# Optimization experiments

Hardware: AMD Instinct MI355X
Metric: run time of the kernel (lower is better)

The kernel has to match this reference:

```python
import jax, jax.numpy as jnp
import numpy as np

MASKED = True


def setup_inputs() -> dict:
    key = jax.random.key(0)
    kq, kk, kv = jax.random.split(key, 3)
    shape = (4, 16, 2048, 64)  # [B, H, S, d]
    q = jax.random.normal(kq, shape, dtype=jnp.float32)
    k = jax.random.normal(kk, shape, dtype=jnp.float32)
    v = jax.random.normal(kv, shape, dtype=jnp.float32)
    return {"q": q, "k": k, "v": v}


def reference(q, k, v):
    d = k.shape[-1]
    scale = 1.0 / jnp.sqrt(jnp.asarray(d, dtype=q.dtype))
    # [B, H, S, S]
    att = jnp.einsum("bhqd,bhkd->bhqk", q, k) * scale
    if MASKED:
        # Faithful to torch source: tril of the scores, then mask where zero
        tri = jnp.tril(att)
        att = jnp.where(tri == 0, -jnp.inf, att)
    att = jax.nn.softmax(att, axis=-1)
    return jnp.einsum("bhqk,bhkd->bhqd", att, v)
```

## Files before the change

### kernel.cpp

```cpp
#include <hip/hip_runtime.h>
#include <hip/hip_bf16.h>

typedef __attribute__((ext_vector_type(8)))  short bf16x8;
typedef __attribute__((ext_vector_type(4)))  float f32x4;
typedef __attribute__((ext_vector_type(16))) float f32x16;
typedef unsigned short ushort_t;

#define S_LEN 2048
#define D_DIM 64
#define FIXED_M 14.0f

#if __has_builtin(__builtin_amdgcn_exp2f)
#define EXP2(x) __builtin_amdgcn_exp2f(x)
#else
#define EXP2(x) __expf((x) * 0.6931471805599453f)
#endif

__device__ __forceinline__ short f2bf(float f) {
  union { float f; unsigned u; } x; x.f = f;
  unsigned r = x.u + 0x7fffu + ((x.u >> 16) & 1u);
  return (short)(r >> 16);
}

__device__ __forceinline__ unsigned cvtpk_bf16(float lo, float hi) {
  unsigned r;
  asm("v_cvt_pk_bf16_f32 %0, %1, %2" : "=v"(r) : "v"(lo), "v"(hi));
  return r;
}

__device__ __forceinline__ void pl32swap(unsigned& a, unsigned& b) {
  asm volatile("v_permlane32_swap_b32 %0, %1" : "+v"(a), "+v"(b));
}

__device__ __forceinline__ void gl_lds16(const ushort_t* g, ushort_t* l) {
  __builtin_amdgcn_global_load_lds(
      (const __attribute__((address_space(1))) unsigned*)g,
      (__attribute__((address_space(3))) unsigned*)l, 16, 0, 0);
}

__global__ void conv_bf16_kernel(const float* __restrict__ in,
                                 ushort_t* __restrict__ out, long n8) {
  long i = (long)blockIdx.x * blockDim.x + threadIdx.x;
  const long stride = (long)gridDim.x * blockDim.x;
  for (; i < n8; i += stride) {
    const float4* p = (const float4*)(in + i * 8);
    float4 a = p[0], b = p[1];
    bf16x8 t;
    t[0]=f2bf(a.x); t[1]=f2bf(a.y); t[2]=f2bf(a.z); t[3]=f2bf(a.w);
    t[4]=f2bf(b.x); t[5]=f2bf(b.y); t[6]=f2bf(b.z); t[7]=f2bf(b.w);
    *(bf16x8*)(out + i * 8) = t;
  }
}

__global__ void transpose_v_kernel(const float* __restrict__ V,
                                   ushort_t* __restrict__ Vt) {
  const int h  = blockIdx.x >> 5;
  const int s0 = (blockIdx.x & 31) * 64;
  const float* Vh = V + (size_t)h * S_LEN * D_DIM;
  ushort_t* Vth   = Vt + (size_t)h * D_DIM * S_LEN;
  __shared__ float tile[64][65];
  const int r  = threadIdx.x >> 2;
  const int c4 = (threadIdx.x & 3) * 16;
#pragma unroll
  for (int j = 0; j < 16; j += 4) {
    float4 x = *(const float4*)(Vh + (size_t)(s0 + r) * D_DIM + c4 + j);
    tile[r][c4 + j + 0] = x.x; tile[r][c4 + j + 1] = x.y;
    tile[r][c4 + j + 2] = x.z; tile[r][c4 + j + 3] = x.w;
  }
  __syncthreads();
  bf16x8 o0, o1;
#pragma unroll
  for (int j = 0; j < 8; ++j) o0[j] = f2bf(tile[c4 + j][r]);
#pragma unroll
  for (int j = 0; j < 8; ++j) o1[j] = f2bf(tile[c4 + 8 + j][r]);
  *(bf16x8*)(Vth + (size_t)r * S_LEN + s0 + c4)     = o0;
  *(bf16x8*)(Vth + (size_t)r * S_LEN + s0 + c4 + 8) = o1;
}

__global__ __launch_bounds__(256, 2)
void flash32_kernel(const float* __restrict__ Qf, const ushort_t* __restrict__ Kb,
                    const ushort_t* __restrict__ Vt, float* __restrict__ Og) {
  const int tid = threadIdx.x;
  const int l   = tid & 63;
  const int wv  = tid >> 6;
  const int hi  = l >> 5;
  const int l31 = l & 31;
  const int l7  = l & 7;
  const int l8  = l >> 3;

  const int bid  = blockIdx.x;
  const int r6   = bid & 63;
  const int head = (r6 & 7) * 8 + (r6 >> 3);
  const int g4   = bid >> 6;
  const int lo2  = g4 & 3;
  const int odd  = (g4 >> 2) & 1;
  const int top  = g4 >> 3;
  const int qidx = odd ? (top * 4 + lo2) : ((15 - top * 4) - lo2);
  const int q0   = qidx * 128;
  const int nt   = 2 * qidx + 2;

  const float*    Qh = Qf + (size_t)head * S_LEN * D_DIM;
  const ushort_t* Kh = Kb + (size_t)head * S_LEN * D_DIM;
  const ushort_t* Vh = Vt + (size_t)head * D_DIM * S_LEN;
  float*          Oh = Og + (size_t)head * S_LEN * D_DIM;

  __shared__ ushort_t smK[4][64 * 64];
  __shared__ ushort_t smV[4][64 * 64];

  const int qrow  = q0 + wv * 32 + l31;
  const int qminw = q0 + wv * 32;

  const int swsrc = (l7 ^ l8) * 8;
  const int rb    = l31 * 64;

#define STAGE_K(T) do {                                                    \
    const int kvk_ = (T) * 64;                                             \
    ushort_t* dst_ = smK[(T) & 3];                                         \
    _Pragma("unroll")                                                      \
    for (int u_ = 0; u_ < 2; ++u_) {                                       \
      const int idx_ = wv * 2 + u_;                                        \
      const int row_ = idx_ * 8 + l8;                                      \
      gl_lds16(Kh + (size_t)(kvk_ + row_) * 64 + swsrc,                    \
               dst_ + idx_ * 512);                                         \
    }                                                                      \
  } while (0)

#define STAGE_V(T) do {                                                    \
    const int kvv_ = (T) * 64;                                             \
    ushort_t* dst_ = smV[(T) & 3];                                         \
    _Pragma("unroll")                                                      \
    for (int u_ = 0; u_ < 2; ++u_) {                                       \
      const int idx_ = wv * 2 + u_;                                        \
      const int d_ = idx_ * 8 + l8;                                        \
      gl_lds16(Vh + (size_t)d_ * S_LEN + kvv_ + swsrc,                     \
               dst_ + idx_ * 512);                                         \
    }                                                                      \
  } while (0)

#define VMCNT0() asm volatile("s_waitcnt vmcnt(0)" ::: "memory")

#define QKT(S0, S1, T) do {                                                \
    _Pragma("unroll")                                                      \
    for (int i = 0; i < 16; ++i) { S0[i] = 0.f; S1[i] = 0.f; }             \
    const ushort_t* kb_ = smK[(T) & 3];                                    \
    __builtin_amdgcn_s_setprio(1);                                         \
    _Pragma("unroll")                                                      \
    for (int ks = 0; ks < 4; ++ks) {                                       \
      const int ch = ((ks * 2 + hi) ^ l7) * 8;                             \
      bf16x8 a0 = *(const bf16x8*)(kb_ + rb + ch);                         \
      bf16x8 a1 = *(const bf16x8*)(kb_ + 2048 + rb + ch);                  \
      S0 = __builtin_amdgcn_mfma_f32_32x32x16_bf16(a0, qf[ks], S0, 0, 0, 0); \
      S1 = __builtin_amdgcn_mfma_f32_32x32x16_bf16(a1, qf[ks], S1, 0, 0, 0); \
    }                                                                      \
    __builtin_amdgcn_s_setprio(0);                                         \
  } while (0)

#define SOFTMAX(S0, S1, KV0, PW) do {                                      \
    if ((KV0) + 63 > qminw) {                                              \
      _Pragma("unroll")                                                    \
      for (int r = 0; r < 16; ++r) {                                       \
        const int crow = (r & 3) + 8 * (r >> 2) + 4 * hi;                  \
        if ((KV0) + crow > qrow)      S0[r] = -INFINITY;                   \
        if ((KV0) + 32 + crow > qrow) S1[r] = -INFINITY;                   \
      }                                                                    \
    }                                                                      \
    _Pragma("unroll")                                                      \
    for (int i = 0; i < 16; ++i) S0[i] = EXP2(S0[i] - FIXED_M);            \
    _Pragma("unroll")                                                      \
    for (int i = 0; i < 16; ++i) S1[i] = EXP2(S1[i] - FIXED_M);            \
    float b8[8];                                                           \
    _Pragma("unroll")                                                      \
    for (int i = 0; i < 8; ++i)                                            \
      b8[i] = (S0[i] + S0[i+8]) + (S1[i] + S1[i+8]);                       \
    _Pragma("unroll")                                                      \
    for (int i = 0; i < 4; ++i) b8[i] += b8[i+4];                          \
    l_run += (b8[0] + b8[2]) + (b8[1] + b8[3]);                            \
    _Pragma("unroll")                                                      \
    for (int ks = 0; ks < 4; ++ks) {                                       \
      const int r0 = (ks & 1) * 8;                                         \
      unsigned w0, w1, w2, w3;                                             \
      if (ks < 2) {                                                        \
        w0 = cvtpk_bf16(S0[r0+0], S0[r0+1]); w2 = cvtpk_bf16(S0[r0+4], S0[r0+5]); \
        w1 = cvtpk_bf16(S0[r0+2], S0[r0+3]); w3 = cvtpk_bf16(S0[r0+6], S0[r0+7]); \
      } else {                                                             \
        w0 = cvtpk_bf16(S1[r0+0], S1[r0+1]); w2 = cvtpk_bf16(S1[r0+4], S1[r0+5]); \
        w1 = cvtpk_bf16(S1[r0+2], S1[r0+3]); w3 = cvtpk_bf16(S1[r0+6], S1[r0+7]); \
      }                                                                    \
      pl32swap(w0, w2); pl32swap(w1, w3);                                  \
      union { unsigned u[4]; bf16x8 v; } pu_;                              \
      pu_.u[0] = w0; pu_.u[1] = w1; pu_.u[2] = w2; pu_.u[3] = w3;          \
      PW[ks] = pu_.v;                                                      \
    }                                                                      \
  } while (0)

#define PV(T, PW) do {                                                     \
    const ushort_t* vb_ = smV[(T) & 3];                                    \
    __builtin_amdgcn_s_setprio(1);                                         \
    _Pragma("unroll")                                                      \
    for (int ks = 0; ks < 4; ++ks) {                                       \
      const int ch = ((ks * 2 + hi) ^ l7) * 8;                             \
      bf16x8 va  = *(const bf16x8*)(vb_ + rb + ch);                        \
      bf16x8 vB2 = *(const bf16x8*)(vb_ + 2048 + rb + ch);                 \
      accA = __builtin_amdgcn_mfma_f32_32x32x16_bf16(va,  PW[ks], accA, 0, 0, 0); \
      accB = __builtin_amdgcn_mfma_f32_32x32x16_bf16(vB2, PW[ks], accB, 0, 0, 0); \
    }                                                                      \
    __builtin_amdgcn_s_setprio(0);                                         \
  } while (0)

  STAGE_K(0);
  STAGE_V(0);
  STAGE_K(1);
  STAGE_V(1);

  bf16x8 qf[4];
  {
    const float sc = 0.125f * 1.44269504089f;
    const float* qp = Qh + (size_t)qrow * D_DIM + 8 * hi;
#pragma unroll
    for (int ks = 0; ks < 4; ++ks) {
      float4 x = *(const float4*)(qp + ks * 16);
      float4 y = *(const float4*)(qp + ks * 16 + 4);
      bf16x8 t;
      t[0]=f2bf(x.x*sc); t[1]=f2bf(x.y*sc);
      t[2]=f2bf(x.z*sc); t[3]=f2bf(x.w*sc);
      t[4]=f2bf(y.x*sc); t[5]=f2bf(y.y*sc);
      t[6]=f2bf(y.z*sc); t[7]=f2bf(y.w*sc);
      qf[ks] = t;
    }
  }

  f32x16 accA, accB, sA0, sA1, sB0, sB1;
#pragma unroll
  for (int i = 0; i < 16; ++i) { accA[i] = 0.f; accB[i] = 0.f; }
  float l_run = 0.f;
  bf16x8 pwA[4], pwB[4];

  VMCNT0();
  __builtin_amdgcn_s_barrier();

  for (int t = 0; t < nt; t += 2) {
    if (t + 2 < nt) {
      STAGE_K(t + 2);
      STAGE_V(t + 2);
      STAGE_K(t + 3);
      STAGE_V(t + 3);
    }
    QKT(sA0, sA1, t);
    QKT(sB0, sB1, t + 1);
    SOFTMAX(sA0, sA1, t * 64, pwA);
    SOFTMAX(sB0, sB1, (t + 1) * 64, pwB);
    PV(t, pwA);
    PV(t + 1, pwB);
    VMCNT0();
    __builtin_amdgcn_s_barrier();
  }

#undef STAGE_K
#undef STAGE_V
#undef VMCNT0
#undef QKT
#undef SOFTMAX
#undef PV

  l_run += __shfl_xor(l_run, 32, 64);
  const float inv = 1.0f / l_run;
  float* op = Oh + (size_t)qrow * D_DIM + 4 * hi;
#pragma unroll
  for (int m4 = 0; m4 < 4; ++m4) {
    float4 a = { accA[4*m4+0]*inv, accA[4*m4+1]*inv,
                 accA[4*m4+2]*inv, accA[4*m4+3]*inv };
    *(float4*)(op + 8 * m4) = a;
    float4 b = { accB[4*m4+0]*inv, accB[4*m4+1]*inv,
                 accB[4*m4+2]*inv, accB[4*m4+3]*inv };
    *(float4*)(op + 32 + 8 * m4) = b;
  }
}

#define BQ 64
#define BK 64
#define LDK 72
#define LDP 72

__device__ __forceinline__ unsigned pack_bf(float lo, float hi) {
  return (unsigned)(unsigned short)f2bf(lo) |
         ((unsigned)(unsigned short)f2bf(hi) << 16);
}

__global__ __launch_bounds__(256, 2)
void flash_fwd_kernel(const float* __restrict__ Qg, const float* __restrict__ Kg,
                      const float* __restrict__ Vg, float* __restrict__ Og) {
  const int tid  = threadIdx.x;
  const int lane = tid & 63;
  const int wv   = tid >> 6;
  const int grp  = lane >> 4;
  const int l16  = lane & 15;
  const int bid = blockIdx.x;
  const int qb  = 31 - (bid & 31);
  const int bh  = bid >> 5;
  const int q0  = qb * BQ;
  const size_t hoff = (size_t)bh * S_LEN * D_DIM;
  const float* Qh = Qg + hoff;
  const float* Kh = Kg + hoff;
  const float* Vh = Vg + hoff;
  float*       Oh = Og + hoff;
  __shared__ short sK [BK][LDK];
  __shared__ short sVT[D_DIM][LDP];
  __shared__ short sP [4][16][LDP];
  bf16x8 qf[2];
  {
    const float* qrow = Qh + (size_t)(q0 + wv*16 + l16) * D_DIM + grp*8;
#pragma unroll
    for (int kc = 0; kc < 2; ++kc) {
      float4 a = *reinterpret_cast<const float4*>(qrow + kc*32);
      float4 b = *reinterpret_cast<const float4*>(qrow + kc*32 + 4);
      bf16x8 t;
      t[0]=f2bf(a.x*0.125f); t[1]=f2bf(a.y*0.125f);
      t[2]=f2bf(a.z*0.125f); t[3]=f2bf(a.w*0.125f);
      t[4]=f2bf(b.x*0.125f); t[5]=f2bf(b.y*0.125f);
      t[6]=f2bf(b.z*0.125f); t[7]=f2bf(b.w*0.125f);
      qf[kc] = t;
    }
  }
  f32x4 acc[4];
#pragma unroll
  for (int nb = 0; nb < 4; ++nb) acc[nb] = (f32x4){0.f, 0.f, 0.f, 0.f};
  float m_i[4] = {-INFINITY, -INFINITY, -INFINITY, -INFINITY};
  float l_i[4] = {0.f, 0.f, 0.f, 0.f};
  const int srow = tid >> 2;
  const int scb  = tid & 3;
  for (int kt = 0; kt <= qb; ++kt) {
    const int kv0 = kt * BK;
    __syncthreads();
    {
      const float* src = Kh + (size_t)(kv0 + srow) * D_DIM + scb*16;
      float4 x0 = *reinterpret_cast<const float4*>(src);
      float4 x1 = *reinterpret_cast<const float4*>(src + 4);
      float4 x2 = *reinterpret_cast<const float4*>(src + 8);
      float4 x3 = *reinterpret_cast<const float4*>(src + 12);
      bf16x8 lo, hi;
      lo[0]=f2bf(x0.x); lo[1]=f2bf(x0.y); lo[2]=f2bf(x0.z); lo[3]=f2bf(x0.w);
      lo[4]=f2bf(x1.x); lo[5]=f2bf(x1.y); lo[6]=f2bf(x1.z); lo[7]=f2bf(x1.w);
      hi[0]=f2bf(x2.x); hi[1]=f2bf(x2.y); hi[2]=f2bf(x2.z); hi[3]=f2bf(x2.w);
      hi[4]=f2bf(x3.x); hi[5]=f2bf(x3.y); hi[6]=f2bf(x3.z); hi[7]=f2bf(x3.w);
      *reinterpret_cast<bf16x8*>(&sK[srow][scb*16])     = lo;
      *reinterpret_cast<bf16x8*>(&sK[srow][scb*16 + 8]) = hi;
    }
    {
      const float* src = Vh + (size_t)(kv0 + scb*16) * D_DIM + srow;
      bf16x8 lo, hi;
#pragma unroll
      for (int j = 0; j < 8; ++j) lo[j] = f2bf(src[(size_t)j * D_DIM]);
#pragma unroll
      for (int j = 0; j < 8; ++j) hi[j] = f2bf(src[(size_t)(j + 8) * D_DIM]);
      *reinterpret_cast<bf16x8*>(&sVT[srow][scb*16])     = lo;
      *reinterpret_cast<bf16x8*>(&sVT[srow][scb*16 + 8]) = hi;
    }
    __syncthreads();
    f32x4 sc[4];
#pragma unroll
    for (int nb = 0; nb < 4; ++nb) {
      f32x4 c = (f32x4){0.f, 0.f, 0.f, 0.f};
#pragma unroll
      for (int kc = 0; kc < 2; ++kc) {
        bf16x8 kf = *reinterpret_cast<const bf16x8*>(&sK[nb*16 + l16][kc*32 + grp*8]);
        c = __builtin_amdgcn_mfma_f32_16x16x32_bf16(qf[kc], kf, c, 0, 0, 0);
      }
      sc[nb] = c;
    }
    const bool diag = (kt == qb);
#pragma unroll
    for (int r = 0; r < 4; ++r) {
      const int qi = wv*16 + grp*4 + r;
      float s0 = sc[0][r], s1 = sc[1][r], s2 = sc[2][r], s3 = sc[3][r];
      if (diag) {
        if (l16 +  0 > qi) s0 = -INFINITY;
        if (l16 + 16 > qi) s1 = -INFINITY;
        if (l16 + 32 > qi) s2 = -INFINITY;
        if (l16 + 48 > qi) s3 = -INFINITY;
      }
      float mx = fmaxf(fmaxf(s0, s1), fmaxf(s2, s3));
#pragma unroll
      for (int off = 8; off; off >>= 1)
        mx = fmaxf(mx, __shfl_xor(mx, off, 64));
      const float mn    = fmaxf(m_i[r], mx);
      const float alpha = __expf(m_i[r] - mn);
      const float p0 = __expf(s0 - mn);
      const float p1 = __expf(s1 - mn);
      const float p2 = __expf(s2 - mn);
      const float p3 = __expf(s3 - mn);
      float rs = (p0 + p1) + (p2 + p3);
#pragma unroll
      for (int off = 8; off; off >>= 1)
        rs += __shfl_xor(rs, off, 64);
      l_i[r] = l_i[r] * alpha + rs;
      m_i[r] = mn;
      acc[0][r] *= alpha; acc[1][r] *= alpha;
      acc[2][r] *= alpha; acc[3][r] *= alpha;
      const float n0 = __shfl_xor(p0, 1, 64);
      const float n1 = __shfl_xor(p1, 1, 64);
      const float n2 = __shfl_xor(p2, 1, 64);
      const float n3 = __shfl_xor(p3, 1, 64);
      if (!(lane & 1)) {
        const int prow = grp*4 + r;
        unsigned* base = reinterpret_cast<unsigned*>(&sP[wv][prow][l16]);
        base[0]  = pack_bf(p0, n0);
        base[8]  = pack_bf(p1, n1);
        base[16] = pack_bf(p2, n2);
        base[24] = pack_bf(p3, n3);
      }
    }
    bf16x8 pf[2];
#pragma unroll
    for (int kc = 0; kc < 2; ++kc)
      pf[kc] = *reinterpret_cast<const bf16x8*>(&sP[wv][l16][kc*32 + grp*8]);
#pragma unroll
    for (int nb = 0; nb < 4; ++nb) {
#pragma unroll
      for (int kc = 0; kc < 2; ++kc) {
        bf16x8 vf = *reinterpret_cast<const bf16x8*>(&sVT[l16 + 16*nb][kc*32 + grp*8]);
        acc[nb] = __builtin_amdgcn_mfma_f32_16x16x32_bf16(pf[kc], vf, acc[nb], 0, 0, 0);
      }
    }
  }
#pragma unroll
  for (int r = 0; r < 4; ++r) {
    const float inv = 1.0f / l_i[r];
    float* orow = Oh + (size_t)(q0 + wv*16 + grp*4 + r) * D_DIM + l16;
#pragma unroll
    for (int nb = 0; nb < 4; ++nb)
      orow[nb*16] = acc[nb][r] * inv;
  }
}

extern "C" void kernel_launch(void* const* d_in, const int* in_sizes, int n_in,
                              void* d_out, int out_size, void* d_ws, size_t ws_size,
                              hipStream_t stream) {
  (void)n_in; (void)out_size;
  const float* q = (const float*)d_in[0];
  const float* k = (const float*)d_in[1];
  const float* v = (const float*)d_in[2];
  float* o = (float*)d_out;
  const int bh = in_sizes[0] / (S_LEN * D_DIM);
  const size_t elems = (size_t)bh * S_LEN * D_DIM;

  if (ws_size >= elems * 2 * 2) {
    ushort_t* Kb = (ushort_t*)d_ws;
    ushort_t* Vt = Kb + elems;
    const long n8 = (long)(elems / 8);
    conv_bf16_kernel<<<2048, 256, 0, stream>>>(k, Kb, n8);
    transpose_v_kernel<<<bh * (S_LEN / 64), 256, 0, stream>>>(v, Vt);
    flash32_kernel<<<bh * (S_LEN / 128), 256, 0, stream>>>(q, Kb, Vt, o);
  } else {
    flash_fwd_kernel<<<bh * (S_LEN / BQ), 256, 0, stream>>>(q, k, v, o);
  }
}
```

Before: 80.86 us.

## Restructure flash kernel into paired causal tiles with software-pipelined QK/softmax/PV

Each block now has 2 waves (128 threads) and handles two 64-row query tiles, tile 31-p and tile p, one after the other, so every block does the same amount of causal work. LDS staging shrinks from 4 to 2 buffers. The loop is software-pipelined so that the next tile's QK^T MFMA runs while the current tile's softmax and PV run, with barriers in between. The fixed max offset is folded into the initial value of the score accumulator, which removes a subtract from the softmax. The trade-off is fewer waves per block, more barriers and serial segments, and the same grid count with half-size blocks.

```diff
diff --git a/kernel.cpp b/kernel.cpp
--- a/kernel.cpp
+++ b/kernel.cpp
@@ -77,7 +77,7 @@
   *(bf16x8*)(Vth + (size_t)r * S_LEN + s0 + c4 + 8) = o1;
 }
 
-__global__ __launch_bounds__(256, 2)
+__global__ __launch_bounds__(128, 2)
 void flash32_kernel(const float* __restrict__ Qf, const ushort_t* __restrict__ Kb,
                     const ushort_t* __restrict__ Vt, float* __restrict__ Og) {
   const int tid = threadIdx.x;
@@ -91,58 +91,52 @@
   const int bid  = blockIdx.x;
   const int r6   = bid & 63;
   const int head = (r6 & 7) * 8 + (r6 >> 3);
-  const int g4   = bid >> 6;
-  const int lo2  = g4 & 3;
-  const int odd  = (g4 >> 2) & 1;
-  const int top  = g4 >> 3;
-  const int qidx = odd ? (top * 4 + lo2) : ((15 - top * 4) - lo2);
-  const int q0   = qidx * 128;
-  const int nt   = 2 * qidx + 2;
+  const int p    = bid >> 6;
+  const int qa   = 31 - p;
+  const int qb   = p;
 
   const float*    Qh = Qf + (size_t)head * S_LEN * D_DIM;
   const ushort_t* Kh = Kb + (size_t)head * S_LEN * D_DIM;
   const ushort_t* Vh = Vt + (size_t)head * D_DIM * S_LEN;
   float*          Oh = Og + (size_t)head * S_LEN * D_DIM;
 
-  __shared__ ushort_t smK[4][64 * 64];
-  __shared__ ushort_t smV[4][64 * 64];
-
-  const int qrow  = q0 + wv * 32 + l31;
-  const int qminw = q0 + wv * 32;
+  __shared__ ushort_t smK[2][64 * 64];
+  __shared__ ushort_t smV[2][64 * 64];
 
   const int swsrc = (l7 ^ l8) * 8;
   const int rb    = l31 * 64;
 
 #define STAGE_K(T) do {                                                    \
     const int kvk_ = (T) * 64;                                             \
-    ushort_t* dst_ = smK[(T) & 3];                                         \
-    _Pragma("unroll")                                                      \
-    for (int u_ = 0; u_ < 2; ++u_) {                                       \
-      const int idx_ = wv * 2 + u_;                                        \
+    ushort_t* dstk_ = smK[(T) & 1];                                        \
+    _Pragma("unroll")                                                      \
+    for (int u_ = 0; u_ < 4; ++u_) {                                       \
+      const int idx_ = wv * 4 + u_;                                        \
       const int row_ = idx_ * 8 + l8;                                      \
       gl_lds16(Kh + (size_t)(kvk_ + row_) * 64 + swsrc,                    \
-               dst_ + idx_ * 512);                                         \
+               dstk_ + idx_ * 512);                                        \
     }                                                                      \
   } while (0)
 
 #define STAGE_V(T) do {                                                    \
     const int kvv_ = (T) * 64;                                             \
-    ushort_t* dst_ = smV[(T) & 3];                                         \
-    _Pragma("unroll")                                                      \
-    for (int u_ = 0; u_ < 2; ++u_) {                                       \
-      const int idx_ = wv * 2 + u_;                                        \
+    ushort_t* dstv_ = smV[(T) & 1];                                        \
+    _Pragma("unroll")                                                      \
+    for (int u_ = 0; u_ < 4; ++u_) {                                       \
+      const int idx_ = wv * 4 + u_;                                        \
       const int d_ = idx_ * 8 + l8;                                        \
       gl_lds16(Vh + (size_t)d_ * S_LEN + kvv_ + swsrc,                     \
-               dst_ + idx_ * 512);                                         \
+               dstv_ + idx_ * 512);                                        \
     }                                                                      \
   } while (0)
 
 #define VMCNT0() asm volatile("s_waitcnt vmcnt(0)" ::: "memory")
+#define BAR()    __builtin_amdgcn_s_barrier()
 
 #define QKT(S0, S1, T) do {                                                \
     _Pragma("unroll")                                                      \
-    for (int i = 0; i < 16; ++i) { S0[i] = 0.f; S1[i] = 0.f; }             \
-    const ushort_t* kb_ = smK[(T) & 3];                                    \
+    for (int i = 0; i < 16; ++i) { S0[i] = -FIXED_M; S1[i] = -FIXED_M; }   \
+    const ushort_t* kb_ = smK[(T) & 1];                                    \
     __builtin_amdgcn_s_setprio(1);                                         \
     _Pragma("unroll")                                                      \
     for (int ks = 0; ks < 4; ++ks) {                                       \
@@ -155,7 +149,7 @@
     __builtin_amdgcn_s_setprio(0);                                         \
   } while (0)
 
-#define SOFTMAX(S0, S1, KV0, PW) do {                                      \
+#define SOFTMAX(S0, S1, KV0) do {                                          \
     if ((KV0) + 63 > qminw) {                                              \
       _Pragma("unroll")                                                    \
       for (int r = 0; r < 16; ++r) {                                       \
@@ -165,9 +159,9 @@
       }                                                                    \
     }                                                                      \
     _Pragma("unroll")                                                      \
-    for (int i = 0; i < 16; ++i) S0[i] = EXP2(S0[i] - FIXED_M);            \
-    _Pragma("unroll")                                                      \
-    for (int i = 0; i < 16; ++i) S1[i] = EXP2(S1[i] - FIXED_M);            \
+    for (int i = 0; i < 16; ++i) S0[i] = EXP2(S0[i]);                      \
+    _Pragma("unroll")                                                      \
+    for (int i = 0; i < 16; ++i) S1[i] = EXP2(S1[i]);                      \
     float b8[8];                                                           \
     _Pragma("unroll")                                                      \
     for (int i = 0; i < 8; ++i)                                            \
@@ -189,91 +183,116 @@
       pl32swap(w0, w2); pl32swap(w1, w3);                                  \
       union { unsigned u[4]; bf16x8 v; } pu_;                              \
       pu_.u[0] = w0; pu_.u[1] = w1; pu_.u[2] = w2; pu_.u[3] = w3;          \
-      PW[ks] = pu_.v;                                                      \
+      pw[ks] = pu_.v;                                                      \
     }                                                                      \
   } while (0)
 
-#define PV(T, PW) do {                                                     \
-    const ushort_t* vb_ = smV[(T) & 3];                                    \
+#define PV(T) do {                                                         \
+    const ushort_t* vb_ = smV[(T) & 1];                                    \
     __builtin_amdgcn_s_setprio(1);                                         \
     _Pragma("unroll")                                                      \
     for (int ks = 0; ks < 4; ++ks) {                                       \
       const int ch = ((ks * 2 + hi) ^ l7) * 8;                             \
       bf16x8 va  = *(const bf16x8*)(vb_ + rb + ch);                        \
       bf16x8 vB2 = *(const bf16x8*)(vb_ + 2048 + rb + ch);                 \
-      accA = __builtin_amdgcn_mfma_f32_32x32x16_bf16(va,  PW[ks], accA, 0, 0, 0); \
-      accB = __builtin_amdgcn_mfma_f32_32x32x16_bf16(vB2, PW[ks], accB, 0, 0, 0); \
+      accA = __builtin_amdgcn_mfma_f32_32x32x16_bf16(va,  pw[ks], accA, 0, 0, 0); \
+      accB = __builtin_amdgcn_mfma_f32_32x32x16_bf16(vB2, pw[ks], accB, 0, 0, 0); \
     }                                                                      \
     __builtin_amdgcn_s_setprio(0);                                         \
   } while (0)
 
-  STAGE_K(0);
-  STAGE_V(0);
-  STAGE_K(1);
-  STAGE_V(1);
-
-  bf16x8 qf[4];
-  {
-    const float sc = 0.125f * 1.44269504089f;
-    const float* qp = Qh + (size_t)qrow * D_DIM + 8 * hi;
-#pragma unroll
-    for (int ks = 0; ks < 4; ++ks) {
-      float4 x = *(const float4*)(qp + ks * 16);
-      float4 y = *(const float4*)(qp + ks * 16 + 4);
-      bf16x8 t;
-      t[0]=f2bf(x.x*sc); t[1]=f2bf(x.y*sc);
-      t[2]=f2bf(x.z*sc); t[3]=f2bf(x.w*sc);
-      t[4]=f2bf(y.x*sc); t[5]=f2bf(y.y*sc);
-      t[6]=f2bf(y.z*sc); t[7]=f2bf(y.w*sc);
-      qf[ks] = t;
-    }
-  }
-
-  f32x16 accA, accB, sA0, sA1, sB0, sB1;
-#pragma unroll
-  for (int i = 0; i < 16; ++i) { accA[i] = 0.f; accB[i] = 0.f; }
-  float l_run = 0.f;
-  bf16x8 pwA[4], pwB[4];
-
-  VMCNT0();
-  __builtin_amdgcn_s_barrier();
-
-  for (int t = 0; t < nt; t += 2) {
-    if (t + 2 < nt) {
+  for (int seg = 0; seg < 2; ++seg) {
+    const int qidx = seg ? qb : qa;
+    const int q0   = qidx * 64;
+    const int nt   = qidx + 1;
+
+    const int qrow  = q0 + wv * 32 + l31;
+    const int qminw = q0 + wv * 32;
+
+    if (seg) BAR();
+
+    STAGE_K(0);
+    STAGE_V(0);
+    STAGE_K(1);
+
+    bf16x8 qf[4];
+    {
+      const float sc = 0.125f * 1.44269504089f;
+      const float* qp = Qh + (size_t)qrow * D_DIM + 8 * hi;
+#pragma unroll
+      for (int ks = 0; ks < 4; ++ks) {
+        float4 x = *(const float4*)(qp + ks * 16);
+        float4 y = *(const float4*)(qp + ks * 16 + 4);
+        bf16x8 t;
+        t[0]=f2bf(x.x*sc); t[1]=f2bf(x.y*sc);
+        t[2]=f2bf(x.z*sc); t[3]=f2bf(x.w*sc);
+        t[4]=f2bf(y.x*sc); t[5]=f2bf(y.y*sc);
+        t[6]=f2bf(y.z*sc); t[7]=f2bf(y.w*sc);
+        qf[ks] = t;
+      }
+    }
+
+    f32x16 accA, accB, sA0, sA1, sB0, sB1;
+#pragma unroll
+    for (int i = 0; i < 16; ++i) { accA[i] = 0.f; accB[i] = 0.f; }
+    float l_run = 0.f;
+    bf16x8 pw[4];
+
+    VMCNT0();
+    BAR();
+    QKT(sA0, sA1, 0);
+
+    int t = 0;
+    for (; t + 2 < nt; t += 2) {
+      VMCNT0(); BAR();
       STAGE_K(t + 2);
+      STAGE_V(t + 1);
+      QKT(sB0, sB1, t + 1);
+      SOFTMAX(sA0, sA1, t * 64);
+      PV(t);
+      VMCNT0(); BAR();
+      if (t + 3 < nt) STAGE_K(t + 3);
       STAGE_V(t + 2);
-      STAGE_K(t + 3);
-      STAGE_V(t + 3);
-    }
-    QKT(sA0, sA1, t);
-    QKT(sB0, sB1, t + 1);
-    SOFTMAX(sA0, sA1, t * 64, pwA);
-    SOFTMAX(sB0, sB1, (t + 1) * 64, pwB);
-    PV(t, pwA);
-    PV(t + 1, pwB);
-    VMCNT0();
-    __builtin_amdgcn_s_barrier();
+      QKT(sA0, sA1, t + 2);
+      SOFTMAX(sB0, sB1, (t + 1) * 64);
+      PV(t + 1);
+    }
+    if (nt - t == 2) {
+      VMCNT0(); BAR();
+      STAGE_V(t + 1);
+      QKT(sB0, sB1, t + 1);
+      SOFTMAX(sA0, sA1, t * 64);
+      PV(t);
+      VMCNT0(); BAR();
+      SOFTMAX(sB0, sB1, (t + 1) * 64);
+      PV(t + 1);
+    } else {
+      VMCNT0(); BAR();
+      SOFTMAX(sA0, sA1, t * 64);
+      PV(t);
+    }
+
+    l_run += __shfl_xor(l_run, 32, 64);
+    const float inv = 1.0f / l_run;
+    float* op = Oh + (size_t)qrow * D_DIM + 4 * hi;
+#pragma unroll
+    for (int m4 = 0; m4 < 4; ++m4) {
+      float4 a = { accA[4*m4+0]*inv, accA[4*m4+1]*inv,
+                   accA[4*m4+2]*inv, accA[4*m4+3]*inv };
+      *(float4*)(op + 8 * m4) = a;
+      float4 b = { accB[4*m4+0]*inv, accB[4*m4+1]*inv,
+                   accB[4*m4+2]*inv, accB[4*m4+3]*inv };
+      *(float4*)(op + 32 + 8 * m4) = b;
+    }
   }
 
 #undef STAGE_K
 #undef STAGE_V
 #undef VMCNT0
+#undef BAR
 #undef QKT
 #undef SOFTMAX
 #undef PV
-
-  l_run += __shfl_xor(l_run, 32, 64);
-  const float inv = 1.0f / l_run;
-  float* op = Oh + (size_t)qrow * D_DIM + 4 * hi;
-#pragma unroll
-  for (int m4 = 0; m4 < 4; ++m4) {
-    float4 a = { accA[4*m4+0]*inv, accA[4*m4+1]*inv,
-                 accA[4*m4+2]*inv, accA[4*m4+3]*inv };
-    *(float4*)(op + 8 * m4) = a;
-    float4 b = { accB[4*m4+0]*inv, accB[4*m4+1]*inv,
-                 accB[4*m4+2]*inv, accB[4*m4+3]*inv };
-    *(float4*)(op + 32 + 8 * m4) = b;
-  }
 }
 
 #define BQ 64
@@ -449,7 +468,7 @@
     const long n8 = (long)(elems / 8);
     conv_bf16_kernel<<<2048, 256, 0, stream>>>(k, Kb, n8);
     transpose_v_kernel<<<bh * (S_LEN / 64), 256, 0, stream>>>(v, Vt);
-    flash32_kernel<<<bh * (S_LEN / 128), 256, 0, stream>>>(q, Kb, Vt, o);
+    flash32_kernel<<<bh * 16, 128, 0, stream>>>(q, Kb, Vt, o);
   } else {
     flash_fwd_kernel<<<bh * (S_LEN / BQ), 256, 0, stream>>>(q, k, v, o);
   }
```

Measured after the change: 78.42 us. -3.0%, faster.

## Replace LDS-staged 4-wave blocks with single-wave blocks loading K/V directly to registers

Applied to the files above, without the earlier changes.

The flash kernel now launches one 64-thread wave per block, each covering 32 query rows, instead of 256-thread blocks covering 128 rows that shared K/V tiles staged in LDS through global_load_lds. Each wave loads its K and V MFMA fragments straight from global memory into registers, double-buffering K across iterations, and drops all LDS use and barriers. The fixed max offset is folded into the score accumulator's initial value. This removes barrier and LDS traffic and adds many more independent blocks, but each wave now fetches K/V itself, so global/L2 traffic rises roughly fourfold and V loads are no longer prefetched ahead of use.

```diff
diff --git a/kernel.cpp b/kernel.cpp
--- a/kernel.cpp
+++ b/kernel.cpp
@@ -30,12 +30,6 @@
 
 __device__ __forceinline__ void pl32swap(unsigned& a, unsigned& b) {
   asm volatile("v_permlane32_swap_b32 %0, %1" : "+v"(a), "+v"(b));
-}
-
-__device__ __forceinline__ void gl_lds16(const ushort_t* g, ushort_t* l) {
-  __builtin_amdgcn_global_load_lds(
-      (const __attribute__((address_space(1))) unsigned*)g,
-      (__attribute__((address_space(3))) unsigned*)l, 16, 0, 0);
 }
 
 __global__ void conv_bf16_kernel(const float* __restrict__ in,
@@ -77,86 +71,67 @@
   *(bf16x8*)(Vth + (size_t)r * S_LEN + s0 + c4 + 8) = o1;
 }
 
-__global__ __launch_bounds__(256, 2)
+__global__ __launch_bounds__(64, 2)
 void flash32_kernel(const float* __restrict__ Qf, const ushort_t* __restrict__ Kb,
                     const ushort_t* __restrict__ Vt, float* __restrict__ Og) {
-  const int tid = threadIdx.x;
-  const int l   = tid & 63;
-  const int wv  = tid >> 6;
+  const int l   = threadIdx.x & 63;
   const int hi  = l >> 5;
   const int l31 = l & 31;
-  const int l7  = l & 7;
-  const int l8  = l >> 3;
 
   const int bid  = blockIdx.x;
   const int r6   = bid & 63;
   const int head = (r6 & 7) * 8 + (r6 >> 3);
-  const int g4   = bid >> 6;
-  const int lo2  = g4 & 3;
-  const int odd  = (g4 >> 2) & 1;
-  const int top  = g4 >> 3;
-  const int qidx = odd ? (top * 4 + lo2) : ((15 - top * 4) - lo2);
-  const int q0   = qidx * 128;
-  const int nt   = 2 * qidx + 2;
+  const int qidx = 63 - (bid >> 6);
+  const int q0   = qidx * 32;
+  const int nt   = ((qidx * 32 + 31) >> 6) + 1;
 
   const float*    Qh = Qf + (size_t)head * S_LEN * D_DIM;
   const ushort_t* Kh = Kb + (size_t)head * S_LEN * D_DIM;
   const ushort_t* Vh = Vt + (size_t)head * D_DIM * S_LEN;
   float*          Oh = Og + (size_t)head * S_LEN * D_DIM;
 
-  __shared__ ushort_t smK[4][64 * 64];
-  __shared__ ushort_t smV[4][64 * 64];
-
-  const int qrow  = q0 + wv * 32 + l31;
-  const int qminw = q0 + wv * 32;
-
-  const int swsrc = (l7 ^ l8) * 8;
-  const int rb    = l31 * 64;
-
-#define STAGE_K(T) do {                                                    \
-    const int kvk_ = (T) * 64;                                             \
-    ushort_t* dst_ = smK[(T) & 3];                                         \
-    _Pragma("unroll")                                                      \
-    for (int u_ = 0; u_ < 2; ++u_) {                                       \
-      const int idx_ = wv * 2 + u_;                                        \
-      const int row_ = idx_ * 8 + l8;                                      \
-      gl_lds16(Kh + (size_t)(kvk_ + row_) * 64 + swsrc,                    \
-               dst_ + idx_ * 512);                                         \
-    }                                                                      \
+  const int qrow = q0 + l31;
+
+#define LOADK(F, T) do {                                                   \
+    const ushort_t* kp_ = Kh + (size_t)((T) * 64 + l31) * 64 + hi * 8;     \
+    F[0] = *(const bf16x8*)(kp_);                                          \
+    F[1] = *(const bf16x8*)(kp_ + 16);                                     \
+    F[2] = *(const bf16x8*)(kp_ + 32);                                     \
+    F[3] = *(const bf16x8*)(kp_ + 48);                                     \
+    const ushort_t* kq_ = kp_ + 32 * 64;                                   \
+    F[4] = *(const bf16x8*)(kq_);                                          \
+    F[5] = *(const bf16x8*)(kq_ + 16);                                     \
+    F[6] = *(const bf16x8*)(kq_ + 32);                                     \
+    F[7] = *(const bf16x8*)(kq_ + 48);                                     \
   } while (0)
 
-#define STAGE_V(T) do {                                                    \
-    const int kvv_ = (T) * 64;                                             \
-    ushort_t* dst_ = smV[(T) & 3];                                         \
-    _Pragma("unroll")                                                      \
-    for (int u_ = 0; u_ < 2; ++u_) {                                       \
-      const int idx_ = wv * 2 + u_;                                        \
-      const int d_ = idx_ * 8 + l8;                                        \
-      gl_lds16(Vh + (size_t)d_ * S_LEN + kvv_ + swsrc,                     \
-               dst_ + idx_ * 512);                                         \
-    }                                                                      \
+#define LOADV(T) do {                                                      \
+    const ushort_t* vp_ = Vh + (size_t)l31 * S_LEN + (T) * 64 + hi * 8;    \
+    vv[0] = *(const bf16x8*)(vp_);                                         \
+    vv[1] = *(const bf16x8*)(vp_ + 16);                                    \
+    vv[2] = *(const bf16x8*)(vp_ + 32);                                    \
+    vv[3] = *(const bf16x8*)(vp_ + 48);                                    \
+    const ushort_t* vq_ = vp_ + (size_t)32 * S_LEN;                        \
+    vv[4] = *(const bf16x8*)(vq_);                                         \
+    vv[5] = *(const bf16x8*)(vq_ + 16);                                    \
+    vv[6] = *(const bf16x8*)(vq_ + 32);                                    \
+    vv[7] = *(const bf16x8*)(vq_ + 48);                                    \
   } while (0)
 
-#define VMCNT0() asm volatile("s_waitcnt vmcnt(0)" ::: "memory")
-
-#define QKT(S0, S1, T) do {                                                \
-    _Pragma("unroll")                                                      \
-    for (int i = 0; i < 16; ++i) { S0[i] = 0.f; S1[i] = 0.f; }             \
-    const ushort_t* kb_ = smK[(T) & 3];                                    \
+#define QKT(F) do {                                                        \
+    _Pragma("unroll")                                                      \
+    for (int i = 0; i < 16; ++i) { S0[i] = -FIXED_M; S1[i] = -FIXED_M; }   \
     __builtin_amdgcn_s_setprio(1);                                         \
     _Pragma("unroll")                                                      \
     for (int ks = 0; ks < 4; ++ks) {                                       \
-      const int ch = ((ks * 2 + hi) ^ l7) * 8;                             \
-      bf16x8 a0 = *(const bf16x8*)(kb_ + rb + ch);                         \
-      bf16x8 a1 = *(const bf16x8*)(kb_ + 2048 + rb + ch);                  \
-      S0 = __builtin_amdgcn_mfma_f32_32x32x16_bf16(a0, qf[ks], S0, 0, 0, 0); \
-      S1 = __builtin_amdgcn_mfma_f32_32x32x16_bf16(a1, qf[ks], S1, 0, 0, 0); \
+      S0 = __builtin_amdgcn_mfma_f32_32x32x16_bf16(F[ks],     qf[ks], S0, 0, 0, 0); \
+      S1 = __builtin_amdgcn_mfma_f32_32x32x16_bf16(F[ks + 4], qf[ks], S1, 0, 0, 0); \
     }                                                                      \
     __builtin_amdgcn_s_setprio(0);                                         \
   } while (0)
 
-#define SOFTMAX(S0, S1, KV0, PW) do {                                      \
-    if ((KV0) + 63 > qminw) {                                              \
+#define SOFTMAX(KV0) do {                                                  \
+    if ((KV0) + 63 > q0) {                                                 \
       _Pragma("unroll")                                                    \
       for (int r = 0; r < 16; ++r) {                                       \
         const int crow = (r & 3) + 8 * (r >> 2) + 4 * hi;                  \
@@ -165,9 +140,9 @@
       }                                                                    \
     }                                                                      \
     _Pragma("unroll")                                                      \
-    for (int i = 0; i < 16; ++i) S0[i] = EXP2(S0[i] - FIXED_M);            \
-    _Pragma("unroll")                                                      \
-    for (int i = 0; i < 16; ++i) S1[i] = EXP2(S1[i] - FIXED_M);            \
+    for (int i = 0; i < 16; ++i) S0[i] = EXP2(S0[i]);                      \
+    _Pragma("unroll")                                                      \
+    for (int i = 0; i < 16; ++i) S1[i] = EXP2(S1[i]);                      \
     float b8[8];                                                           \
     _Pragma("unroll")                                                      \
     for (int i = 0; i < 8; ++i)                                            \
@@ -189,28 +164,19 @@
       pl32swap(w0, w2); pl32swap(w1, w3);                                  \
       union { unsigned u[4]; bf16x8 v; } pu_;                              \
       pu_.u[0] = w0; pu_.u[1] = w1; pu_.u[2] = w2; pu_.u[3] = w3;          \
-      PW[ks] = pu_.v;                                                      \
+      pw[ks] = pu_.v;                                                      \
     }                                                                      \
   } while (0)
 
-#define PV(T, PW) do {                                                     \
-    const ushort_t* vb_ = smV[(T) & 3];                                    \
+#define PV() do {                                                          \
     __builtin_amdgcn_s_setprio(1);                                         \
     _Pragma("unroll")                                                      \
     for (int ks = 0; ks < 4; ++ks) {                                       \
-      const int ch = ((ks * 2 + hi) ^ l7) * 8;                             \
-      bf16x8 va  = *(const bf16x8*)(vb_ + rb + ch);                        \
-      bf16x8 vB2 = *(const bf16x8*)(vb_ + 2048 + rb + ch);                 \
-      accA = __builtin_amdgcn_mfma_f32_32x32x16_bf16(va,  PW[ks], accA, 0, 0, 0); \
-      accB = __builtin_amdgcn_mfma_f32_32x32x16_bf16(vB2, PW[ks], accB, 0, 0, 0); \
+      accA = __builtin_amdgcn_mfma_f32_32x32x16_bf16(vv[ks],     pw[ks], accA, 0, 0, 0); \
+      accB = __builtin_amdgcn_mfma_f32_32x32x16_bf16(vv[ks + 4], pw[ks], accB, 0, 0, 0); \
     }                                                                      \
     __builtin_amdgcn_s_setprio(0);                                         \
   } while (0)
-
-  STAGE_K(0);
-  STAGE_V(0);
-  STAGE_K(1);
-  STAGE_V(1);
 
   bf16x8 qf[4];
   {
@@ -229,35 +195,38 @@
     }
   }
 
-  f32x16 accA, accB, sA0, sA1, sB0, sB1;
+  f32x16 accA, accB, S0, S1;
 #pragma unroll
   for (int i = 0; i < 16; ++i) { accA[i] = 0.f; accB[i] = 0.f; }
   float l_run = 0.f;
-  bf16x8 pwA[4], pwB[4];
-
-  VMCNT0();
-  __builtin_amdgcn_s_barrier();
-
-  for (int t = 0; t < nt; t += 2) {
-    if (t + 2 < nt) {
-      STAGE_K(t + 2);
-      STAGE_V(t + 2);
-      STAGE_K(t + 3);
-      STAGE_V(t + 3);
-    }
-    QKT(sA0, sA1, t);
-    QKT(sB0, sB1, t + 1);
-    SOFTMAX(sA0, sA1, t * 64, pwA);
-    SOFTMAX(sB0, sB1, (t + 1) * 64, pwB);
-    PV(t, pwA);
-    PV(t + 1, pwB);
-    VMCNT0();
-    __builtin_amdgcn_s_barrier();
-  }
-
-#undef STAGE_K
-#undef STAGE_V
-#undef VMCNT0
+  bf16x8 ka[8], kb2[8], vv[8], pw[4];
+
+  LOADK(ka, 0);
+
+  int t = 0;
+  while (true) {
+    {
+      const int kv0 = t * 64;
+      LOADV(t);
+      if (t + 1 < nt) LOADK(kb2, t + 1);
+      QKT(ka);
+      SOFTMAX(kv0);
+      PV();
+    }
+    if (++t >= nt) break;
+    {
+      const int kv0 = t * 64;
+      LOADV(t);
+      if (t + 1 < nt) LOADK(ka, t + 1);
+      QKT(kb2);
+      SOFTMAX(kv0);
+      PV();
+    }
+    if (++t >= nt) break;
+  }
+
+#undef LOADK
+#undef LOADV
 #undef QKT
 #undef SOFTMAX
 #undef PV
@@ -449,7 +418,7 @@
     const long n8 = (long)(elems / 8);
     conv_bf16_kernel<<<2048, 256, 0, stream>>>(k, Kb, n8);
     transpose_v_kernel<<<bh * (S_LEN / 64), 256, 0, stream>>>(v, Vt);
-    flash32_kernel<<<bh * (S_LEN / 128), 256, 0, stream>>>(q, Kb, Vt, o);
+    flash32_kernel<<<bh * 64, 64, 0, stream>>>(q, Kb, Vt, o);
   } else {
     flash_fwd_kernel<<<bh * (S_LEN / BQ), 256, 0, stream>>>(q, k, v, o);
   }
```

After: 149.8 us. +85.3%, slower.

## Pair causal query tiles per block and merge prep kernels into one launch

Applied to the files above, without the earlier changes.

Each attention block now processes two query tiles, one heavy (15-p) and one light (p), so every block does the same total causal work. The grid shrinks from 1024 to 512 blocks. The K conversion and V transpose are merged into a single prep kernel launch. The fixed max offset is folded into the accumulator initialisation, which removes one subtract per exp. The cost is less block-level parallelism and serial segments inside each block, and the fast path now also requires exactly 64 heads.

```diff
diff --git a/kernel.cpp b/kernel.cpp
--- a/kernel.cpp
+++ b/kernel.cpp
@@ -38,43 +38,44 @@
       (__attribute__((address_space(3))) unsigned*)l, 16, 0, 0);
 }
 
-__global__ void conv_bf16_kernel(const float* __restrict__ in,
-                                 ushort_t* __restrict__ out, long n8) {
-  long i = (long)blockIdx.x * blockDim.x + threadIdx.x;
-  const long stride = (long)gridDim.x * blockDim.x;
-  for (; i < n8; i += stride) {
-    const float4* p = (const float4*)(in + i * 8);
-    float4 a = p[0], b = p[1];
-    bf16x8 t;
-    t[0]=f2bf(a.x); t[1]=f2bf(a.y); t[2]=f2bf(a.z); t[3]=f2bf(a.w);
-    t[4]=f2bf(b.x); t[5]=f2bf(b.y); t[6]=f2bf(b.z); t[7]=f2bf(b.w);
-    *(bf16x8*)(out + i * 8) = t;
-  }
-}
-
-__global__ void transpose_v_kernel(const float* __restrict__ V,
-                                   ushort_t* __restrict__ Vt) {
-  const int h  = blockIdx.x >> 5;
-  const int s0 = (blockIdx.x & 31) * 64;
-  const float* Vh = V + (size_t)h * S_LEN * D_DIM;
-  ushort_t* Vth   = Vt + (size_t)h * D_DIM * S_LEN;
-  __shared__ float tile[64][65];
-  const int r  = threadIdx.x >> 2;
-  const int c4 = (threadIdx.x & 3) * 16;
-#pragma unroll
-  for (int j = 0; j < 16; j += 4) {
-    float4 x = *(const float4*)(Vh + (size_t)(s0 + r) * D_DIM + c4 + j);
-    tile[r][c4 + j + 0] = x.x; tile[r][c4 + j + 1] = x.y;
-    tile[r][c4 + j + 2] = x.z; tile[r][c4 + j + 3] = x.w;
-  }
-  __syncthreads();
-  bf16x8 o0, o1;
-#pragma unroll
-  for (int j = 0; j < 8; ++j) o0[j] = f2bf(tile[c4 + j][r]);
-#pragma unroll
-  for (int j = 0; j < 8; ++j) o1[j] = f2bf(tile[c4 + 8 + j][r]);
-  *(bf16x8*)(Vth + (size_t)r * S_LEN + s0 + c4)     = o0;
-  *(bf16x8*)(Vth + (size_t)r * S_LEN + s0 + c4 + 8) = o1;
+__global__ void prep_kernel(const float* __restrict__ Kf, const float* __restrict__ Vf,
+                            ushort_t* __restrict__ Kb, ushort_t* __restrict__ Vt) {
+  if (blockIdx.x < 2048) {
+    const long n8 = (long)64 * S_LEN * D_DIM / 8;
+    long i = (long)blockIdx.x * blockDim.x + threadIdx.x;
+    const long stride = (long)2048 * blockDim.x;
+    for (; i < n8; i += stride) {
+      const float4* p = (const float4*)(Kf + i * 8);
+      float4 a = p[0], b = p[1];
+      bf16x8 t;
+      t[0]=f2bf(a.x); t[1]=f2bf(a.y); t[2]=f2bf(a.z); t[3]=f2bf(a.w);
+      t[4]=f2bf(b.x); t[5]=f2bf(b.y); t[6]=f2bf(b.z); t[7]=f2bf(b.w);
+      *(bf16x8*)(Kb + i * 8) = t;
+    }
+  } else {
+    const int bid = blockIdx.x - 2048;
+    const int h  = bid >> 5;
+    const int s0 = (bid & 31) * 64;
+    const float* Vh = Vf + (size_t)h * S_LEN * D_DIM;
+    ushort_t* Vth   = Vt + (size_t)h * D_DIM * S_LEN;
+    __shared__ float tile[64][65];
+    const int r  = threadIdx.x >> 2;
+    const int c4 = (threadIdx.x & 3) * 16;
+#pragma unroll
+    for (int j = 0; j < 16; j += 4) {
+      float4 x = *(const float4*)(Vh + (size_t)(s0 + r) * D_DIM + c4 + j);
+      tile[r][c4 + j + 0] = x.x; tile[r][c4 + j + 1] = x.y;
+      tile[r][c4 + j + 2] = x.z; tile[r][c4 + j + 3] = x.w;
+    }
+    __syncthreads();
+    bf16x8 o0, o1;
+#pragma unroll
+    for (int j = 0; j < 8; ++j) o0[j] = f2bf(tile[c4 + j][r]);
+#pragma unroll
+    for (int j = 0; j < 8; ++j) o1[j] = f2bf(tile[c4 + 8 + j][r]);
+    *(bf16x8*)(Vth + (size_t)r * S_LEN + s0 + c4)     = o0;
+    *(bf16x8*)(Vth + (size_t)r * S_LEN + s0 + c4 + 8) = o1;
+  }
 }
 
 __global__ __launch_bounds__(256, 2)
@@ -91,13 +92,9 @@
   const int bid  = blockIdx.x;
   const int r6   = bid & 63;
   const int head = (r6 & 7) * 8 + (r6 >> 3);
-  const int g4   = bid >> 6;
-  const int lo2  = g4 & 3;
-  const int odd  = (g4 >> 2) & 1;
-  const int top  = g4 >> 3;
-  const int qidx = odd ? (top * 4 + lo2) : ((15 - top * 4) - lo2);
-  const int q0   = qidx * 128;
-  const int nt   = 2 * qidx + 2;
+  const int p    = bid >> 6;
+  const int qhiQ = 15 - p;
+  const int qloQ = p;
 
   const float*    Qh = Qf + (size_t)head * S_LEN * D_DIM;
   const ushort_t* Kh = Kb + (size_t)head * S_LEN * D_DIM;
@@ -107,41 +104,37 @@
   __shared__ ushort_t smK[4][64 * 64];
   __shared__ ushort_t smV[4][64 * 64];
 
-  const int qrow  = q0 + wv * 32 + l31;
-  const int qminw = q0 + wv * 32;
-
   const int swsrc = (l7 ^ l8) * 8;
   const int rb    = l31 * 64;
 
 #define STAGE_K(T) do {                                                    \
     const int kvk_ = (T) * 64;                                             \
-    ushort_t* dst_ = smK[(T) & 3];                                         \
+    ushort_t* dk_ = smK[(T) & 3];                                          \
     _Pragma("unroll")                                                      \
     for (int u_ = 0; u_ < 2; ++u_) {                                       \
       const int idx_ = wv * 2 + u_;                                        \
       const int row_ = idx_ * 8 + l8;                                      \
-      gl_lds16(Kh + (size_t)(kvk_ + row_) * 64 + swsrc,                    \
-               dst_ + idx_ * 512);                                         \
+      gl_lds16(Kh + (size_t)(kvk_ + row_) * 64 + swsrc, dk_ + idx_ * 512); \
     }                                                                      \
   } while (0)
 
 #define STAGE_V(T) do {                                                    \
     const int kvv_ = (T) * 64;                                             \
-    ushort_t* dst_ = smV[(T) & 3];                                         \
+    ushort_t* dv_ = smV[(T) & 3];                                          \
     _Pragma("unroll")                                                      \
     for (int u_ = 0; u_ < 2; ++u_) {                                       \
       const int idx_ = wv * 2 + u_;                                        \
       const int d_ = idx_ * 8 + l8;                                        \
-      gl_lds16(Vh + (size_t)d_ * S_LEN + kvv_ + swsrc,                     \
-               dst_ + idx_ * 512);                                         \
+      gl_lds16(Vh + (size_t)d_ * S_LEN + kvv_ + swsrc, dv_ + idx_ * 512);  \
     }                                                                      \
   } while (0)
 
 #define VMCNT0() asm volatile("s_waitcnt vmcnt(0)" ::: "memory")
+#define BAR()    __builtin_amdgcn_s_barrier()
 
 #define QKT(S0, S1, T) do {                                                \
     _Pragma("unroll")                                                      \
-    for (int i = 0; i < 16; ++i) { S0[i] = 0.f; S1[i] = 0.f; }             \
+    for (int i = 0; i < 16; ++i) { S0[i] = -FIXED_M; S1[i] = -FIXED_M; }   \
     const ushort_t* kb_ = smK[(T) & 3];                                    \
     __builtin_amdgcn_s_setprio(1);                                         \
     _Pragma("unroll")                                                      \
@@ -165,9 +158,9 @@
       }                                                                    \
     }                                                                      \
     _Pragma("unroll")                                                      \
-    for (int i = 0; i < 16; ++i) S0[i] = EXP2(S0[i] - FIXED_M);            \
-    _Pragma("unroll")                                                      \
-    for (int i = 0; i < 16; ++i) S1[i] = EXP2(S1[i] - FIXED_M);            \
+    for (int i = 0; i < 16; ++i) S0[i] = EXP2(S0[i]);                      \
+    _Pragma("unroll")                                                      \
+    for (int i = 0; i < 16; ++i) S1[i] = EXP2(S1[i]);                      \
     float b8[8];                                                           \
     _Pragma("unroll")                                                      \
     for (int i = 0; i < 8; ++i)                                            \
@@ -207,73 +200,83 @@
     __builtin_amdgcn_s_setprio(0);                                         \
   } while (0)
 
-  STAGE_K(0);
-  STAGE_V(0);
-  STAGE_K(1);
-  STAGE_V(1);
-
-  bf16x8 qf[4];
-  {
-    const float sc = 0.125f * 1.44269504089f;
-    const float* qp = Qh + (size_t)qrow * D_DIM + 8 * hi;
-#pragma unroll
-    for (int ks = 0; ks < 4; ++ks) {
-      float4 x = *(const float4*)(qp + ks * 16);
-      float4 y = *(const float4*)(qp + ks * 16 + 4);
-      bf16x8 t;
-      t[0]=f2bf(x.x*sc); t[1]=f2bf(x.y*sc);
-      t[2]=f2bf(x.z*sc); t[3]=f2bf(x.w*sc);
-      t[4]=f2bf(y.x*sc); t[5]=f2bf(y.y*sc);
-      t[6]=f2bf(y.z*sc); t[7]=f2bf(y.w*sc);
-      qf[ks] = t;
-    }
-  }
-
-  f32x16 accA, accB, sA0, sA1, sB0, sB1;
-#pragma unroll
-  for (int i = 0; i < 16; ++i) { accA[i] = 0.f; accB[i] = 0.f; }
-  float l_run = 0.f;
-  bf16x8 pwA[4], pwB[4];
-
-  VMCNT0();
-  __builtin_amdgcn_s_barrier();
-
-  for (int t = 0; t < nt; t += 2) {
-    if (t + 2 < nt) {
-      STAGE_K(t + 2);
-      STAGE_V(t + 2);
-      STAGE_K(t + 3);
-      STAGE_V(t + 3);
-    }
-    QKT(sA0, sA1, t);
-    QKT(sB0, sB1, t + 1);
-    SOFTMAX(sA0, sA1, t * 64, pwA);
-    SOFTMAX(sB0, sB1, (t + 1) * 64, pwB);
-    PV(t, pwA);
-    PV(t + 1, pwB);
+  for (int seg = 0; seg < 2; ++seg) {
+    const int qidx = seg ? qloQ : qhiQ;
+    const int q0   = qidx * 128;
+    const int nt   = 2 * qidx + 2;
+
+    const int qrow  = q0 + wv * 32 + l31;
+    const int qminw = q0 + wv * 32;
+
+    STAGE_K(0);
+    STAGE_V(0);
+    STAGE_K(1);
+    STAGE_V(1);
+
+    bf16x8 qf[4];
+    {
+      const float sc = 0.125f * 1.44269504089f;
+      const float* qp = Qh + (size_t)qrow * D_DIM + 8 * hi;
+#pragma unroll
+      for (int ks = 0; ks < 4; ++ks) {
+        float4 x = *(const float4*)(qp + ks * 16);
+        float4 y = *(const float4*)(qp + ks * 16 + 4);
+        bf16x8 t;
+        t[0]=f2bf(x.x*sc); t[1]=f2bf(x.y*sc);
+        t[2]=f2bf(x.z*sc); t[3]=f2bf(x.w*sc);
+        t[4]=f2bf(y.x*sc); t[5]=f2bf(y.y*sc);
+        t[6]=f2bf(y.z*sc); t[7]=f2bf(y.w*sc);
+        qf[ks] = t;
+      }
+    }
+
+    f32x16 accA, accB, sA0, sA1, sB0, sB1;
+#pragma unroll
+    for (int i = 0; i < 16; ++i) { accA[i] = 0.f; accB[i] = 0.f; }
+    float l_run = 0.f;
+    bf16x8 pwA[4], pwB[4];
+
     VMCNT0();
-    __builtin_amdgcn_s_barrier();
+    BAR();
+
+    for (int t = 0; t < nt; t += 2) {
+      if (t + 2 < nt) {
+        STAGE_K(t + 2);
+        STAGE_V(t + 2);
+        STAGE_K(t + 3);
+        STAGE_V(t + 3);
+      }
+      QKT(sA0, sA1, t);
+      QKT(sB0, sB1, t + 1);
+      SOFTMAX(sA0, sA1, t * 64, pwA);
+      SOFTMAX(sB0, sB1, (t + 1) * 64, pwB);
+      PV(t, pwA);
+      PV(t + 1, pwB);
+      VMCNT0();
+      BAR();
+    }
+
+    l_run += __shfl_xor(l_run, 32, 64);
+    const float inv = 1.0f / l_run;
+    float* op = Oh + (size_t)qrow * D_DIM + 4 * hi;
+#pragma unroll
+    for (int m4 = 0; m4 < 4; ++m4) {
+      float4 a = { accA[4*m4+0]*inv, accA[4*m4+1]*inv,
+                   accA[4*m4+2]*inv, accA[4*m4+3]*inv };
+      *(float4*)(op + 8 * m4) = a;
+      float4 b = { accB[4*m4+0]*inv, accB[4*m4+1]*inv,
+                   accB[4*m4+2]*inv, accB[4*m4+3]*inv };
+      *(float4*)(op + 32 + 8 * m4) = b;
+    }
   }
 
 #undef STAGE_K
 #undef STAGE_V
 #undef VMCNT0
+#undef BAR
 #undef QKT
 #undef SOFTMAX
 #undef PV
-
-  l_run += __shfl_xor(l_run, 32, 64);
-  const float inv = 1.0f / l_run;
-  float* op = Oh + (size_t)qrow * D_DIM + 4 * hi;
-#pragma unroll
-  for (int m4 = 0; m4 < 4; ++m4) {
-    float4 a = { accA[4*m4+0]*inv, accA[4*m4+1]*inv,
-                 accA[4*m4+2]*inv, accA[4*m4+3]*inv };
-    *(float4*)(op + 8 * m4) = a;
-    float4 b = { accB[4*m4+0]*inv, accB[4*m4+1]*inv,
-                 accB[4*m4+2]*inv, accB[4*m4+3]*inv };
-    *(float4*)(op + 32 + 8 * m4) = b;
-  }
 }
 
 #define BQ 64
@@ -443,13 +446,11 @@
   const int bh = in_sizes[0] / (S_LEN * D_DIM);
   const size_t elems = (size_t)bh * S_LEN * D_DIM;
 
-  if (ws_size >= elems * 2 * 2) {
+  if (ws_size >= elems * 2 * 2 && bh == 64) {
     ushort_t* Kb = (ushort_t*)d_ws;
     ushort_t* Vt = Kb + elems;
-    const long n8 = (long)(elems / 8);
-    conv_bf16_kernel<<<2048, 256, 0, stream>>>(k, Kb, n8);
-    transpose_v_kernel<<<bh * (S_LEN / 64), 256, 0, stream>>>(v, Vt);
-    flash32_kernel<<<bh * (S_LEN / 128), 256, 0, stream>>>(q, Kb, Vt, o);
+    prep_kernel<<<4096, 256, 0, stream>>>(k, v, Kb, Vt);
+    flash32_kernel<<<bh * 8, 256, 0, stream>>>(q, Kb, Vt, o);
   } else {
     flash_fwd_kernel<<<bh * (S_LEN / BQ), 256, 0, stream>>>(q, k, v, o);
   }
```

Result: faster. 72.32 us (-10.6%).
